# Kernel optimization log

Hardware: AMD Instinct MI355X
Metric: run time of the kernel (lower is better)

## Reference

```python
import jax, jax.numpy as jnp
import numpy as np
from jax import lax

B, CIN, HID, H, W, PS = 16, 64, 64, 128, 128, 8
PH, PW = H // PS, W // PS          # patch grid (16,16)
N = PH * PW                        # 256 patch tokens


def setup_inputs() -> dict:
    key = jax.random.key(0)
    ks = jax.random.split(key, 16)

    def wn(k, shape, s=0.02):
        return jax.random.normal(k, shape, jnp.float32) * s

    z = lambda n: jnp.zeros((n,), jnp.float32)
    return {
        "x": jax.random.normal(ks[0], (B, CIN, H, W), jnp.float32),
        "c": jax.random.normal(ks[1], (B, HID, H, W), jnp.float32),
        "h": jax.random.normal(ks[2], (B, HID, H, W), jnp.float32),
        "m": jax.random.normal(ks[3], (B, HID, H, W), jnp.float32),
        "conv_w": wn(ks[4], (4 * HID, CIN + HID, 3, 3)), "conv_b": z(4 * HID),
        "gn_w": jnp.ones((4 * HID,), jnp.float32), "gn_b": z(4 * HID),
        "qh_w": wn(ks[5], (HID, HID)), "qh_b": z(HID),
        "kh_w": wn(ks[6], (HID, HID)), "kh_b": z(HID),
        "vh_w": wn(ks[7], (HID, HID)), "vh_b": z(HID),
        "km_w": wn(ks[8], (HID, HID)), "km_b": z(HID),
        "vm_w": wn(ks[9], (HID, HID)), "vm_b": z(HID),
        "z_w": wn(ks[10], (2 * HID, 2 * HID)), "z_b": z(2 * HID),
        "m_w": wn(ks[11], (3 * HID, 3 * HID)), "m_b": z(3 * HID),
    }


def _conv1x1(t, w, b):
    return jnp.einsum('bchw,oc->bohw', t, w) + b[None, :, None, None]


def _pool(t):
    # Faithful to torch: view(B,C,N,-1).mean(-1) on row-major flattened HW
    b, c = t.shape[:2]
    return t.reshape(b, c, N, -1).mean(-1)  # (B,C,N)


def _cell(x, c, h, m, conv_w, conv_b, gn_w, gn_b,
          qh_w, qh_b, kh_w, kh_b, vh_w, vh_b, km_w, km_b, vm_w, vm_b,
          z_w, z_b, m_w, m_b):
    # --- ConvLSTM gating: 3x3 conv + GroupNorm(groups == channels) ---
    comb = jnp.concatenate([x, h], axis=1)
    cc = lax.conv_general_dilated(comb, conv_w, (1, 1), 'SAME',
                                  dimension_numbers=('NCHW', 'OIHW', 'NCHW'))
    cc = cc + conv_b[None, :, None, None]
    mu = cc.mean((2, 3), keepdims=True)
    var = cc.var((2, 3), keepdims=True)
    cc = (cc - mu) * lax.rsqrt(var + 1e-5)
    cc = cc * gn_w[None, :, None, None] + gn_b[None, :, None, None]
    i, f, g, o = jnp.split(cc, 4, axis=1)
    c_next = jax.nn.sigmoid(f) * c + jax.nn.sigmoid(i) * jnp.tanh(g)
    h_next = jax.nn.sigmoid(o) * jnp.tanh(c_next)

    # --- SA memory module ---
    Kp = _pool(_conv1x1(h_next, kh_w, kh_b))          # (B,C,N)
    Qp = _pool(_conv1x1(h_next, qh_w, qh_b))          # (B,C,N)
    Vp = _pool(_conv1x1(h_next, vh_w, vh_b))          # (B,C,N)
    Kmp = _pool(_conv1x1(m, km_w, km_b))
    Vmp = _pool(_conv1x1(m, vm_w, vm_b))

    A_h = jax.nn.softmax(jnp.einsum('bcn,bcm->bnm', Qp, Kp), axis=-1)   # (B,N,N)
    A_m = jax.nn.softmax(jnp.einsum('bcn,bcm->bnm', Qp, Kmp), axis=-1)
    Zh = jnp.einsum('bnm,bcm->bcn', A_h, Vp).reshape(-1, HID, PH, PW)
    Zm = jnp.einsum('bnm,bcm->bcn', A_m, Vmp).reshape(-1, HID, PH, PW)

    # bilinear upsample (half-pixel centers == torch align_corners=False)
    Zh = jax.image.resize(Zh, (Zh.shape[0], HID, H, W), 'bilinear')
    Zm = jax.image.resize(Zm, (Zm.shape[0], HID, H, W), 'bilinear')

    Z = _conv1x1(jnp.concatenate([Zh, Zm], axis=1), z_w, z_b)
    combined = _conv1x1(jnp.concatenate([Z, h_next], axis=1), m_w, m_b)
    mo, mg, mi = jnp.split(combined, 3, axis=1)
    mi = jax.nn.sigmoid(mi)
    new_m = (1 - mi) * m + mi * jnp.tanh(mg)
    new_h = jax.nn.sigmoid(mo) * new_m
    return new_h, c_next, new_m


def reference(x, c, h, m, conv_w, conv_b, gn_w, gn_b,
              qh_w, qh_b, kh_w, kh_b, vh_w, vh_b, km_w, km_b, vm_w, vm_b,
              z_w, z_b, m_w, m_b):
    return _cell(x, c, h, m, conv_w, conv_b, gn_w, gn_b,
                 qh_w, qh_b, kh_w, kh_b, vh_w, vh_b, km_w, km_b, vm_w, vm_b,
                 z_w, z_b, m_w, m_b)
```

## Files before the change

### kernel.cpp

```cpp
#include <hip/hip_runtime.h>
#include <hip/hip_bf16.h>
#include <math.h>

typedef __attribute__((ext_vector_type(4))) float f4;
typedef __attribute__((ext_vector_type(4))) float f32x4;
typedef __attribute__((ext_vector_type(8))) short bf16x8;

#define HSZ 128
#define WSZ 128
#define HW 16384

__device__ __forceinline__ float sigm(float x){ return 1.f/(1.f+__expf(-x)); }
__device__ __forceinline__ float tanh_fast(float x){ return 1.f - 2.f/(1.f+__expf(2.f*x)); }
__device__ __forceinline__ float bf_lo(unsigned u){ return __uint_as_float(u<<16); }
__device__ __forceinline__ float bf_hi(unsigned u){ return __uint_as_float(u & 0xffff0000u); }

__global__ void k_setup(const float* __restrict__ conv_w, const float* __restrict__ m_w,
                        const float* __restrict__ z_w, const float* __restrict__ z_b,
                        const float* __restrict__ m_b,
                        __hip_bfloat16* __restrict__ wB, __hip_bfloat16* __restrict__ WhB,
                        float* __restrict__ W2, float* __restrict__ bc){
  int idx = blockIdx.x*256 + threadIdx.x;
  if (idx < 294912){
    int kk = idx & 31;
    int oc = (idx>>5) & 255;
    int q  = idx >> 13;
    int dx = q % 3; int t2 = q / 3; int ck = t2 & 3; int dy = t2 >> 2;
    int ic = ck*32 + kk;
    wB[idx] = __float2bfloat16(conv_w[((oc*128+ic)*3+dy)*3+dx]);
  } else if (idx < 307200){
    int j = idx - 294912;
    int o = j >> 6, ci = j & 63;
    WhB[j] = __float2bfloat16(m_w[o*192 + 128 + ci]);
  } else if (idx < 331776){
    int j = idx - 307200;
    int o = j >> 7, zi = j & 127;
    float s = 0.f;
    for (int zo=0; zo<128; zo++) s += m_w[o*192+zo]*z_w[zo*128+zi];
    W2[j] = s;
  } else if (idx < 331968){
    int o = idx - 331776;
    float s = m_b[o];
    for (int zo=0; zo<128; zo++) s += m_w[o*192+zo]*z_b[zo];
    bc[o] = s;
  }
}

__global__ __launch_bounds__(256) void k_im(const float* __restrict__ x,
    const float* __restrict__ h, __hip_bfloat16* __restrict__ im, int b0){
  __shared__ __hip_bfloat16 T[128*136];
  int bid = blockIdx.x; int y = bid & 127, bl = bid >> 7; int b = b0 + bl;
  int t = threadIdx.x;
  for (int idx=t; idx<4096; idx+=256){
    int c = idx>>5, xq = idx&31;
    const float* src = (c<64)? x : h; int cm = c&63;
    f4 v = *(const f4*)(src + ((((size_t)b*64+cm)*HSZ + y)*WSZ + xq*4));
    #pragma unroll
    for (int j=0;j<4;j++) T[(xq*4+j)*136 + c] = __float2bfloat16(v[j]);
  }
  __syncthreads();
  for (int idx=t; idx<2048; idx+=256){
    int xx = idx>>4, q = idx&15;
    uint4 v = *(const uint4*)&T[xx*136 + q*8];
    *(uint4*)(im + ((((size_t)bl*HSZ + y)*WSZ + xx)*128 + q*8)) = v;
  }
}

__global__ __launch_bounds__(256) void k_conv(const __hip_bfloat16* __restrict__ im,
    const __hip_bfloat16* __restrict__ wB, __hip_bfloat16* __restrict__ cc, int b0){
  __shared__ __align__(16) short LDS[17408];
  short* buf0 = LDS;
  short* buf1 = LDS + 5280;
  int bid0 = blockIdx.x;
  int cpx = gridDim.x >> 3;
  int bid = (bid0 & 7)*cpx + (bid0 >> 3);
  int y = bid & 127, bl = bid >> 7; int b = b0 + bl;
  int oc0 = blockIdx.y * 128;
  int t = threadIdx.x;
  int lane = t & 63, w = t >> 6;
  int ln15 = lane & 15, h8 = (lane>>4)*8;
  int ocw = (w>>1)*64, pxw = (w&1)*64;
  int px0 = t>>2, q0 = t&3;

  f32x4 acc[4][4];
  #pragma unroll
  for (int mi=0;mi<4;mi++)
    #pragma unroll
    for (int ni=0;ni<4;ni++) acc[mi][ni] = (f32x4){0.f,0.f,0.f,0.f};

  uint4 sv0, sv1, sv2;
  auto stage_load = [&](int s){
    int dy = s>>2, ck = s&3;
    int yy = y + dy - 1;
    bool yok = (yy>=0) && (yy<HSZ);
    const __hip_bfloat16* rb = im + (((size_t)bl*HSZ + yy)*WSZ)*128 + ck*32;
    sv0 = make_uint4(0u,0u,0u,0u);
    sv1 = make_uint4(0u,0u,0u,0u);
    sv2 = make_uint4(0u,0u,0u,0u);
    if (yok && px0>=1)       sv0 = *(const uint4*)(rb + (size_t)(px0-1)*128 + q0*8);
    if (yok)                 sv1 = *(const uint4*)(rb + (size_t)(px0+63)*128 + q0*8);
    if (yok && t<4)          sv2 = *(const uint4*)(rb + (size_t)127*128 + q0*8);
  };
  auto stage_write = [&](short* dst){
    *(uint4*)&dst[px0*40 + q0*8]      = sv0;
    *(uint4*)&dst[(px0+64)*40 + q0*8] = sv1;
    if (t<16) *(uint4*)&dst[(128+(t>>2))*40 + q0*8] = sv2;
  };
  auto ldw = [&](int u, bf16x8 af[4]){
    const __hip_bfloat16* wp = wB + (((size_t)u*256 + oc0 + ocw + ln15)*32 + h8);
    #pragma unroll
    for (int i=0;i<4;i++) af[i] = *(const bf16x8*)(wp + (size_t)i*16*32);
  };

  bf16x8 afc[4];
  stage_load(0); stage_write(buf0);
  ldw(0, afc);
  __syncthreads();
  for (int s=0; s<12; s++){
    short* cur = (s&1)? buf1 : buf0;
    short* nxt = (s&1)? buf0 : buf1;
    if (s < 11) stage_load(s+1);
    #pragma unroll
    for (int dx=0; dx<3; dx++){
      int u = s*3 + dx;
      bf16x8 afn[4];
      bool more = (u < 35);
      if (more) ldw(u+1, afn);
      bf16x8 bfr[4];
      #pragma unroll
      for (int i=0;i<4;i++) bfr[i] = *(const bf16x8*)&cur[(pxw + i*16 + ln15 + dx)*40 + h8];
      #pragma unroll
      for (int mi=0;mi<4;mi++)
        #pragma unroll
        for (int ni=0;ni<4;ni++)
          acc[mi][ni] = __builtin_amdgcn_mfma_f32_16x16x32_bf16(afc[mi], bfr[ni], acc[mi][ni], 0, 0, 0);
      if (more){
        #pragma unroll
        for (int i=0;i<4;i++) afc[i] = afn[i];
      }
    }
    if (s < 11) stage_write(nxt);
    __syncthreads();
  }

  __hip_bfloat16* OutL = (__hip_bfloat16*)LDS;
  int hv4 = (lane>>4)*4;
  #pragma unroll
  for (int mi=0;mi<4;mi++)
    #pragma unroll
    for (int ni=0;ni<4;ni++){
      #pragma unroll
      for (int r=0;r<4;r++)
        OutL[(ocw + mi*16 + hv4 + r)*136 + pxw + ni*16 + ln15] = __float2bfloat16(acc[mi][ni][r]);
    }
  __syncthreads();
  for (int idx=t; idx<2048; idx+=256){
    int oc = idx>>4, qc = idx&15;
    uint4 v = *(const uint4*)&OutL[oc*136 + qc*8];
    *(uint4*)(cc + ((((size_t)b*256 + oc0 + oc)*HSZ + y)*WSZ + qc*8)) = v;
  }
}

__global__ __launch_bounds__(256) void k_gnpool(const __hip_bfloat16* __restrict__ cc,
    const float* __restrict__ gn_w, const float* __restrict__ gn_b,
    float* __restrict__ scale, float* __restrict__ shift,
    const float* __restrict__ m_in, float* __restrict__ poolm){
  int bid = blockIdx.x;
  if (bid < 4096){
    int bc_ = bid;
    const uint4* p = (const uint4*)(cc + (size_t)bc_*HW);
    float s=0.f, ss=0.f;
    for (int ch=threadIdx.x; ch<2048; ch+=256){
      uint4 u = p[ch];
      unsigned uw[4] = {u.x, u.y, u.z, u.w};
      #pragma unroll
      for (int w=0; w<4; w++){
        float a = bf_lo(uw[w]);
        float b2 = bf_hi(uw[w]);
        s += a + b2; ss += a*a + b2*b2;
      }
    }
    for (int off=1; off<64; off<<=1){ s += __shfl_xor(s, off); ss += __shfl_xor(ss, off); }
    __shared__ float rs_[4], rss_[4];
    int wv = threadIdx.x>>6, ln = threadIdx.x&63;
    if (ln==0){ rs_[wv]=s; rss_[wv]=ss; }
    __syncthreads();
    if (threadIdx.x==0){
      float S = rs_[0]+rs_[1]+rs_[2]+rs_[3];
      float SS = rss_[0]+rss_[1]+rss_[2]+rss_[3];
      float mu = S*(1.f/16384.f);
      float var = SS*(1.f/16384.f) - mu*mu;
      float r = rsqrtf(var + 1e-5f);
      int oc = bc_ & 255;
      float sc = gn_w[oc]*r;
      scale[bc_] = sc;
      shift[bc_] = gn_b[oc] - mu*sc;
    }
  } else {
    int pc = bid - 4096;
    const float* src = m_in + (size_t)pc*HW;
    float* dst = poolm + (size_t)pc*256;
    int n = threadIdx.x;
    const f4* p = (const f4*)(src + n*64);
    float s = 0.f;
    #pragma unroll
    for (int i=0;i<16;i++){ f4 v = p[i]; s += (v[0]+v[1]) + (v[2]+v[3]); }
    dst[n] = s*(1.f/64.f);
  }
}

__global__ __launch_bounds__(256) void k_gate(const __hip_bfloat16* __restrict__ cc,
    const float* __restrict__ cin, const float* __restrict__ scale, const float* __restrict__ shift,
    float* __restrict__ out_c, float* __restrict__ out_h, float* __restrict__ poolh){
  int bid = blockIdx.x;
  int b = bid>>6, c = bid&63;
  size_t base_i = ((size_t)b*256 + c)*HW;
  const uint4* pi = (const uint4*)(cc + base_i);
  const uint4* pf = (const uint4*)(cc + base_i + (size_t)64*HW);
  const uint4* pg = (const uint4*)(cc + base_i + (size_t)128*HW);
  const uint4* po = (const uint4*)(cc + base_i + (size_t)192*HW);
  float ssi = scale[b*256+c],     shi = shift[b*256+c];
  float ssf = scale[b*256+64+c],  shf = shift[b*256+64+c];
  float ssg = scale[b*256+128+c], shg = shift[b*256+128+c];
  float sso = scale[b*256+192+c], sho = shift[b*256+192+c];
  size_t pbase = ((size_t)b*64 + c)*HW;
  const f4* pc_ = (const f4*)(cin + pbase);
  f4* oc_ = (f4*)(out_c + pbase);
  f4* oh_ = (f4*)(out_h + pbase);
  int lane = threadIdx.x & 63;
  for (int ch = threadIdx.x; ch < 2048; ch += 256){
    uint4 ui = pi[ch], uf = pf[ch], ug = pg[ch], uo = po[ch];
    unsigned iu[4]={ui.x,ui.y,ui.z,ui.w}, fu[4]={uf.x,uf.y,uf.z,uf.w};
    unsigned gu[4]={ug.x,ug.y,ug.z,ug.w}, ou[4]={uo.x,uo.y,uo.z,uo.w};
    f4 ca = pc_[ch*2], cb = pc_[ch*2+1];
    float cvv[8] = {ca[0],ca[1],ca[2],ca[3],cb[0],cb[1],cb[2],cb[3]};
    float rc[8], rh[8];
    #pragma unroll
    for (int w=0; w<4; w++){
      #pragma unroll
      for (int hl=0; hl<2; hl++){
        int k = w*2+hl;
        float iv = (hl? bf_hi(iu[w]) : bf_lo(iu[w]))*ssi + shi;
        float fv = (hl? bf_hi(fu[w]) : bf_lo(fu[w]))*ssf + shf;
        float gv = (hl? bf_hi(gu[w]) : bf_lo(gu[w]))*ssg + shg;
        float ov = (hl? bf_hi(ou[w]) : bf_lo(ou[w]))*sso + sho;
        float cn = sigm(fv)*cvv[k] + sigm(iv)*tanh_fast(gv);
        rc[k] = cn;
        rh[k] = sigm(ov)*tanh_fast(cn);
      }
    }
    f4 o0 = {rc[0],rc[1],rc[2],rc[3]}, o1 = {rc[4],rc[5],rc[6],rc[7]};
    f4 h0 = {rh[0],rh[1],rh[2],rh[3]}, h1 = {rh[4],rh[5],rh[6],rh[7]};
    oc_[ch*2] = o0; oc_[ch*2+1] = o1;
    oh_[ch*2] = h0; oh_[ch*2+1] = h1;
    float ps = ((rh[0]+rh[1])+(rh[2]+rh[3])) + ((rh[4]+rh[5])+(rh[6]+rh[7]));
    ps += __shfl_xor(ps, 1);
    ps += __shfl_xor(ps, 2);
    ps += __shfl_xor(ps, 4);
    if ((lane & 7) == 0) poolh[(size_t)bid*256 + (ch>>3)] = ps*(1.f/64.f);
  }
}

__global__ __launch_bounds__(256) void k_proj(const float* __restrict__ pool,
    const float* qw,const float* qb,const float* kw,const float* kb,
    const float* vw,const float* vb,const float* kmw,const float* kmb,
    const float* vmw,const float* vmb, float* __restrict__ proj){
  int bid = blockIdx.x;
  int p = bid % 5, b = bid / 5;
  const float* P = pool + (p>=3? 262144:0) + (size_t)b*16384;
  const float* W; const float* Bs;
  if (p==0){W=qw;Bs=qb;} else if(p==1){W=kw;Bs=kb;} else if(p==2){W=vw;Bs=vb;}
  else if (p==3){W=kmw;Bs=kmb;} else {W=vmw;Bs=vmb;}
  int n = threadIdx.x;
  float acc[64];
  #pragma unroll
  for (int o=0;o<64;o++) acc[o]=0.f;
  for (int c=0;c<64;c++){
    float pv = P[c*256+n];
    #pragma unroll
    for (int o=0;o<64;o++) acc[o] += W[o*64+c]*pv;
  }
  float* dst = proj + (size_t)p*262144 + (size_t)b*16384;
  #pragma unroll
  for (int o=0;o<64;o++) dst[o*256+n] = acc[o] + Bs[o];
}

__global__ __launch_bounds__(256) void k_scores(const float* __restrict__ proj, float* __restrict__ A){
  int n = blockIdx.x, ty = blockIdx.y, b = blockIdx.z;
  const float* Q = proj + (size_t)b*16384;
  const float* K = proj + (size_t)(ty==0?1:3)*262144 + (size_t)b*16384;
  int mm = threadIdx.x;
  float s = 0.f;
  for (int c=0;c<64;c++) s += Q[c*256+n]*K[c*256+mm];
  float mx = s;
  for (int off=1; off<64; off<<=1) mx = fmaxf(mx, __shfl_xor(mx, off));
  __shared__ float r1[4], r2[4];
  int wv = threadIdx.x>>6, ln = threadIdx.x&63;
  if (ln==0) r1[wv]=mx;
  __syncthreads();
  mx = fmaxf(fmaxf(r1[0],r1[1]),fmaxf(r1[2],r1[3]));
  float e = __expf(s-mx);
  float sm = e;
  for (int off=1; off<64; off<<=1) sm += __shfl_xor(sm, off);
  if (ln==0) r2[wv]=sm;
  __syncthreads();
  sm = r2[0]+r2[1]+r2[2]+r2[3];
  A[(((size_t)ty*16+b)*256+n)*256+mm] = e/sm;
}

__global__ __launch_bounds__(256) void k_apply(const float* __restrict__ proj,
    const float* __restrict__ A, float* __restrict__ Zcat){
  int ty = blockIdx.x, b = blockIdx.y, cq = blockIdx.z;
  const float* V = proj + (size_t)(ty==0?2:4)*262144 + (size_t)b*16384 + (size_t)cq*16*256;
  const float* Ar = A + (((size_t)ty*16+b)*256 + threadIdx.x)*256;
  float acc[16];
  #pragma unroll
  for (int c=0;c<16;c++) acc[c]=0.f;
  for (int mm=0; mm<256; mm++){
    float a = Ar[mm];
    #pragma unroll
    for (int c=0;c<16;c++) acc[c] += V[c*256+mm]*a;
  }
  float* dst = Zcat + ((size_t)b*128 + ty*64 + cq*16)*256 + threadIdx.x;
  #pragma unroll
  for (int c=0;c<16;c++) dst[c*256] = acc[c];
}

__global__ __launch_bounds__(256) void k_csmall(const float* __restrict__ Zcat,
    const float* __restrict__ W2, float* __restrict__ Cs){
  int oq = blockIdx.x, b = blockIdx.y;
  int o0 = oq*32;
  int n = threadIdx.x;
  float acc[32];
  #pragma unroll
  for (int o=0;o<32;o++) acc[o]=0.f;
  for (int zi=0; zi<128; zi++){
    float z = Zcat[((size_t)b*128+zi)*256 + n];
    #pragma unroll
    for (int o=0;o<32;o++) acc[o] += W2[(o0+o)*128 + zi]*z;
  }
  float* dst = Cs + ((size_t)b*192 + o0)*256 + n;
  #pragma unroll
  for (int o=0;o<32;o++) dst[o*256] = acc[o];
}

__global__ __launch_bounds__(256, 3) void k_final(
    const float* __restrict__ hn, const float* __restrict__ m_in,
    const __hip_bfloat16* __restrict__ WhB, const float* __restrict__ Cs,
    const float* __restrict__ bcv, float* __restrict__ out_h, float* __restrict__ out_m){
  __shared__ float rowF[64*69];
  __shared__ float CsL[192*36];
  int bid = blockIdx.x;
  int xh = bid & 1, y = (bid>>1) & 127, b = bid >> 8;
  int x0 = xh*64;
  int t = threadIdx.x, lane = t & 63, w = t >> 6;
  int ln15 = lane & 15, hi = lane >> 4, h8 = hi*8;

  float sy = (y+0.5f)*0.125f - 0.5f;
  int iy = (int)floorf(sy); float fy = sy - (float)iy;
  int ya = min(max(iy,0),15), yb = min(max(iy+1,0),15);

  for (int idx=t; idx<1024; idx+=256){
    int c = idx>>4, xq = idx&15;
    f4 v = *(const f4*)(hn + ((((size_t)b*64+c)*HSZ + y)*WSZ + x0 + xq*4));
    float* d = &rowF[c*69 + xq*4];
    d[0]=v[0]; d[1]=v[1]; d[2]=v[2]; d[3]=v[3];
  }
  for (int idx=t; idx<1536; idx+=256){
    int cp = idx>>3, rr = (idx>>2)&1, q = idx&3;
    int ry = rr? yb : ya;
    f4 v = *(const f4*)(Cs + (((size_t)b*192 + cp)*256 + ry*16 + q*4));
    *(f4*)&CsL[cp*36 + rr*16 + q*4] = v;
  }
  __syncthreads();

  bf16x8 bfr[2];
  #pragma unroll
  for (int ks=0; ks<2; ks++){
    union { bf16x8 v; __hip_bfloat16 e[8]; } u;
    #pragma unroll
    for (int j=0;j<8;j++)
      u.e[j] = __float2bfloat16(rowF[(ks*32 + h8 + j)*69 + w*16 + ln15]);
    bfr[ks] = u.v;
  }
  f32x4 acc[12];
  #pragma unroll
  for (int mt=0;mt<12;mt++) acc[mt] = (f32x4){0.f,0.f,0.f,0.f};
  #pragma unroll
  for (int ks=0; ks<2; ks++){
    #pragma unroll
    for (int mt=0; mt<12; mt++){
      bf16x8 af = *(const bf16x8*)(WhB + ((mt*16+ln15)*64 + ks*32 + h8));
      acc[mt] = __builtin_amdgcn_mfma_f32_16x16x32_bf16(af, bfr[ks], acc[mt], 0, 0, 0);
    }
  }

  int xg = x0 + w*16 + ln15;
  float sx = (xg+0.5f)*0.125f - 0.5f;
  int ix = (int)floorf(sx); float fx = sx - (float)ix;
  int xa = min(max(ix,0),15), xb2 = min(max(ix+1,0),15);
  float w00=(1.f-fy)*(1.f-fx), w01=(1.f-fy)*fx, w10=fy*(1.f-fx), w11=fy*fx;
  int o00 = xa, o01 = xb2, o10 = 16+xa, o11 = 16+xb2;
  #pragma unroll
  for (int mt=0; mt<4; mt++){
    #pragma unroll
    for (int r=0; r<4; r++){
      int c = mt*16 + hi*4 + r;
      const float* p0 = &CsL[c*36];
      const float* p1 = &CsL[(64+c)*36];
      const float* p2 = &CsL[(128+c)*36];
      float vo = acc[mt][r]   + p0[o00]*w00 + p0[o01]*w01 + p0[o10]*w10 + p0[o11]*w11 + bcv[c];
      float vg = acc[mt+4][r] + p1[o00]*w00 + p1[o01]*w01 + p1[o10]*w10 + p1[o11]*w11 + bcv[64+c];
      float vi = acc[mt+8][r] + p2[o00]*w00 + p2[o01]*w01 + p2[o10]*w10 + p2[o11]*w11 + bcv[128+c];
      size_t pix = (((size_t)b*64+c)*HSZ + y)*WSZ + xg;
      float mv = m_in[pix];
      float smi = sigm(vi);
      float nm = (1.f-smi)*mv + smi*tanh_fast(vg);
      float nh = sigm(vo)*nm;
      out_h[pix] = nh;
      out_m[pix] = nm;
    }
  }
}

extern "C" void kernel_launch(void* const* d_in, const int* in_sizes, int n_in,
                              void* d_out, int out_size, void* d_ws, size_t ws_size,
                              hipStream_t stream){
  (void)in_sizes; (void)n_in; (void)out_size;
  const float* x    = (const float*)d_in[0];
  const float* cst  = (const float*)d_in[1];
  const float* h    = (const float*)d_in[2];
  const float* m    = (const float*)d_in[3];
  const float* conv_w = (const float*)d_in[4];
  const float* gn_w = (const float*)d_in[6];
  const float* gn_b = (const float*)d_in[7];
  const float* qh_w = (const float*)d_in[8];  const float* qh_b = (const float*)d_in[9];
  const float* kh_w = (const float*)d_in[10]; const float* kh_b = (const float*)d_in[11];
  const float* vh_w = (const float*)d_in[12]; const float* vh_b = (const float*)d_in[13];
  const float* km_w = (const float*)d_in[14]; const float* km_b = (const float*)d_in[15];
  const float* vm_w = (const float*)d_in[16]; const float* vm_b = (const float*)d_in[17];
  const float* z_w  = (const float*)d_in[18]; const float* z_b  = (const float*)d_in[19];
  const float* m_w  = (const float*)d_in[20]; const float* m_b  = (const float*)d_in[21];

  float* out   = (float*)d_out;
  float* out_h = out;
  float* out_c = out + 16777216;
  float* out_m = out + 33554432;

  char* ws = (char*)d_ws;
  __hip_bfloat16* cc = (__hip_bfloat16*)ws;
  float* proj = (float*)(ws + 2097152);
  float* Amat = (float*)(ws + 7340032);
  float* Zcat = (float*)(ws + 15728640);
  float* Cs   = (float*)(ws + 17825792);
  float* pool = (float*)(ws + 134217728);

  bool big = (ws_size >= (size_t)202200000);
  size_t imOff = 134217728;
  size_t wOff  = big ? (imOff + 67108864) : 150994944;
  __hip_bfloat16* im  = (__hip_bfloat16*)(ws + imOff);
  __hip_bfloat16* wB  = (__hip_bfloat16*)(ws + wOff);
  __hip_bfloat16* WhB = (__hip_bfloat16*)(ws + wOff +  589824);
  float* W2   = (float*)(ws + wOff +  614400);
  float* bcv  = (float*)(ws + wOff +  712704);
  float* gnsc = (float*)(ws + wOff +  713472);
  float* gnsh = (float*)(ws + wOff +  729856);

  hipLaunchKernelGGL(k_setup, dim3(1297), dim3(256), 0, stream,
                     conv_w, m_w, z_w, z_b, m_b, wB, WhB, W2, bcv);
  if (big){
    hipLaunchKernelGGL(k_im,   dim3(2048),    dim3(256), 0, stream, x, h, im, 0);
    hipLaunchKernelGGL(k_conv, dim3(2048, 2), dim3(256), 0, stream, im, wB, cc, 0);
  } else {
    for (int q = 0; q < 4; q++){
      hipLaunchKernelGGL(k_im,   dim3(512),    dim3(256), 0, stream, x, h, im, q*4);
      hipLaunchKernelGGL(k_conv, dim3(512, 2), dim3(256), 0, stream, im, wB, cc, q*4);
    }
  }
  hipLaunchKernelGGL(k_gnpool, dim3(5120), dim3(256), 0, stream, cc, gn_w, gn_b, gnsc, gnsh,
                     m, pool + 262144);
  hipLaunchKernelGGL(k_gate, dim3(1024), dim3(256), 0, stream, cc, cst, gnsc, gnsh, out_c, out_h, pool);
  hipLaunchKernelGGL(k_proj, dim3(80), dim3(256), 0, stream, pool,
                     qh_w,qh_b,kh_w,kh_b,vh_w,vh_b,km_w,km_b,vm_w,vm_b, proj);
  hipLaunchKernelGGL(k_scores, dim3(256,2,16), dim3(256), 0, stream, proj, Amat);
  hipLaunchKernelGGL(k_apply, dim3(2,16,4), dim3(256), 0, stream, proj, Amat, Zcat);
  hipLaunchKernelGGL(k_csmall, dim3(6,16), dim3(256), 0, stream, Zcat, W2, Cs);
  hipLaunchKernelGGL(k_final, dim3(4096), dim3(256), 0, stream, out_h, m, WhB, Cs, bcv, out_h, out_m);
}
```

Measured before the change: 580.6 us.

## Stage 64 input channels per LDS buffer in conv to halve barrier count

The implicit-GEMM 3x3 conv now stages 64 input channels per row (padded to a 72-short stride) per pipeline stage instead of 32. This cuts the loop from 12 stages to 6, with 6 MFMA sub-steps per stage, halving the number of __syncthreads and global-to-LDS staging rounds. The cost is larger LDS buffers, more registers held for staged loads, and more complex weight-index arithmetic, which could reduce occupancy.

```diff
diff --git a/kernel.cpp b/kernel.cpp
--- a/kernel.cpp
+++ b/kernel.cpp
@@ -68,9 +68,9 @@
 
 __global__ __launch_bounds__(256) void k_conv(const __hip_bfloat16* __restrict__ im,
     const __hip_bfloat16* __restrict__ wB, __hip_bfloat16* __restrict__ cc, int b0){
-  __shared__ __align__(16) short LDS[17408];
+  __shared__ __align__(16) short LDS[18720];
   short* buf0 = LDS;
-  short* buf1 = LDS + 5280;
+  short* buf1 = LDS + 9360;
   int bid0 = blockIdx.x;
   int cpx = gridDim.x >> 3;
   int bid = (bid0 & 7)*cpx + (bid0 >> 3);
@@ -80,7 +80,7 @@
   int lane = t & 63, w = t >> 6;
   int ln15 = lane & 15, h8 = (lane>>4)*8;
   int ocw = (w>>1)*64, pxw = (w&1)*64;
-  int px0 = t>>2, q0 = t&3;
+  int spx = t>>3, sq = t&7;
 
   f32x4 acc[4][4];
   #pragma unroll
@@ -88,23 +88,33 @@
     #pragma unroll
     for (int ni=0;ni<4;ni++) acc[mi][ni] = (f32x4){0.f,0.f,0.f,0.f};
 
-  uint4 sv0, sv1, sv2;
+  uint4 sv[4]; uint4 svt;
   auto stage_load = [&](int s){
-    int dy = s>>2, ck = s&3;
+    int dy = s>>1, c0 = (s&1)*64;
     int yy = y + dy - 1;
     bool yok = (yy>=0) && (yy<HSZ);
-    const __hip_bfloat16* rb = im + (((size_t)bl*HSZ + yy)*WSZ)*128 + ck*32;
-    sv0 = make_uint4(0u,0u,0u,0u);
-    sv1 = make_uint4(0u,0u,0u,0u);
-    sv2 = make_uint4(0u,0u,0u,0u);
-    if (yok && px0>=1)       sv0 = *(const uint4*)(rb + (size_t)(px0-1)*128 + q0*8);
-    if (yok)                 sv1 = *(const uint4*)(rb + (size_t)(px0+63)*128 + q0*8);
-    if (yok && t<4)          sv2 = *(const uint4*)(rb + (size_t)127*128 + q0*8);
+    const __hip_bfloat16* rb = im + (((size_t)bl*HSZ + yy)*WSZ)*128 + c0;
+    #pragma unroll
+    for (int k=0;k<4;k++){
+      int idx = t + k*256;
+      int px = idx>>3, q = idx&7;
+      sv[k] = make_uint4(0u,0u,0u,0u);
+      if (yok && px>=1) sv[k] = *(const uint4*)(rb + (size_t)(px-1)*128 + q*8);
+    }
+    svt = make_uint4(0u,0u,0u,0u);
+    if (yok && t<8) svt = *(const uint4*)(rb + (size_t)127*128 + t*8);
   };
   auto stage_write = [&](short* dst){
-    *(uint4*)&dst[px0*40 + q0*8]      = sv0;
-    *(uint4*)&dst[(px0+64)*40 + q0*8] = sv1;
-    if (t<16) *(uint4*)&dst[(128+(t>>2))*40 + q0*8] = sv2;
+    #pragma unroll
+    for (int k=0;k<4;k++){
+      int idx = t + k*256;
+      int px = idx>>3, q = idx&7;
+      *(uint4*)&dst[px*72 + q*8] = sv[k];
+    }
+    if (t<8){
+      *(uint4*)&dst[128*72 + t*8] = svt;
+      *(uint4*)&dst[129*72 + t*8] = make_uint4(0u,0u,0u,0u);
+    }
   };
   auto ldw = [&](int u, bf16x8 af[4]){
     const __hip_bfloat16* wp = wB + (((size_t)u*256 + oc0 + ocw + ln15)*32 + h8);
@@ -116,19 +126,26 @@
   stage_load(0); stage_write(buf0);
   ldw(0, afc);
   __syncthreads();
-  for (int s=0; s<12; s++){
+  for (int s=0; s<6; s++){
     short* cur = (s&1)? buf1 : buf0;
     short* nxt = (s&1)? buf0 : buf1;
-    if (s < 11) stage_load(s+1);
-    #pragma unroll
-    for (int dx=0; dx<3; dx++){
-      int u = s*3 + dx;
+    if (s < 5) stage_load(s+1);
+    #pragma unroll
+    for (int j=0; j<6; j++){
+      int kh = j&1, dxv = j>>1;
+      int step = s*6 + j;
+      bool more = (step < 35);
       bf16x8 afn[4];
-      bool more = (u < 35);
-      if (more) ldw(u+1, afn);
+      if (more){
+        int jn = (j==5)? 0 : j+1;
+        int sn = (j==5)? s+1 : s;
+        int un = ((sn>>1)*4 + (sn&1)*2 + (jn&1))*3 + (jn>>1);
+        ldw(un, afn);
+      }
       bf16x8 bfr[4];
       #pragma unroll
-      for (int i=0;i<4;i++) bfr[i] = *(const bf16x8*)&cur[(pxw + i*16 + ln15 + dx)*40 + h8];
+      for (int i=0;i<4;i++)
+        bfr[i] = *(const bf16x8*)&cur[(pxw + i*16 + ln15 + dxv)*72 + kh*32 + h8];
       #pragma unroll
       for (int mi=0;mi<4;mi++)
         #pragma unroll
@@ -139,7 +156,7 @@
         for (int i=0;i<4;i++) afc[i] = afn[i];
       }
     }
-    if (s < 11) stage_write(nxt);
+    if (s < 5) stage_write(nxt);
     __syncthreads();
   }
 
```

Result: slower. 596.2 us (+2.7%).
